# Performance work log

Hardware: AMD Instinct MI355X
Metric: run time of the kernel (lower is better)

## Reference

```python
import jax, jax.numpy as jnp
import numpy as np

N_NODES = 100000
N_EDGES = 1600000
IN_DIM = 128
HID_DIM = 128
N_MASK = 5000
N_CLASSES = 4


def gcn_layer(x, src, dst, edge_weight, W, b):
    """PyG GCNConv: x' = D^{-1/2} (A + I) D^{-1/2} (x W) + b, with edge weights."""
    n = x.shape[0]
    loop = jnp.arange(n, dtype=src.dtype)
    s = jnp.concatenate([src, loop])                      # [E+N]
    d = jnp.concatenate([dst, loop])                      # [E+N]
    w = jnp.concatenate([edge_weight, jnp.ones((n,), edge_weight.dtype)])
    deg = jax.ops.segment_sum(w, d, num_segments=n)       # weighted in-degree incl. self-loop
    dis = jnp.where(deg > 0, jax.lax.rsqrt(deg), 0.0)     # deg^{-1/2}, inf -> 0
    norm = dis[s] * w * dis[d]                            # [E+N]
    h = x @ W                                             # [N, H] small GEMM
    msg = h[s] * norm[:, None]                            # gather + scale  [E+N, H]
    out = jax.ops.segment_sum(msg, d, num_segments=n)     # scatter-add     [N, H]
    return out + b


def setup_inputs() -> dict:
    key = jax.random.key(0)
    ks = jax.random.split(key, 8)
    x = jax.random.normal(ks[0], (N_NODES, IN_DIM), dtype=jnp.float32)
    edge_weight = jax.random.uniform(ks[1], (N_EDGES,), dtype=jnp.float32)
    W1 = jax.random.normal(ks[2], (IN_DIM, HID_DIM), dtype=jnp.float32) * (1.0 / np.sqrt(IN_DIM))
    b1 = jnp.zeros((HID_DIM,), jnp.float32)
    W2 = jax.random.normal(ks[3], (HID_DIM, HID_DIM), dtype=jnp.float32) * (1.0 / np.sqrt(HID_DIM))
    b2 = jnp.zeros((HID_DIM,), jnp.float32)
    edge_index = jax.random.randint(ks[4], (2, N_EDGES), 0, N_NODES, dtype=jnp.int32)
    mask_idx = jax.random.randint(ks[5], (N_MASK,), 0, N_NODES, dtype=jnp.int32)
    y = jax.random.randint(ks[6], (N_NODES,), 0, N_CLASSES, dtype=jnp.int32)
    return {"x": x, "edge_weight": edge_weight, "W1": W1, "b1": b1,
            "W2": W2, "b2": b2, "edge_index": edge_index,
            "mask_idx": mask_idx, "y": y}


def reference(x, edge_weight, W1, b1, W2, b2, edge_index, mask_idx, y):
    src, dst = edge_index[0], edge_index[1]
    h = gcn_layer(x, src, dst, edge_weight, W1, b1)
    h = jax.nn.relu(h)
    # F.dropout(training=False) in eval mode is identity
    h = gcn_layer(h, src, dst, edge_weight, W2, b2)
    return h[mask_idx], y[mask_idx]
```

## Files before the change

kernel.cpp:

```cpp
#include <hip/hip_runtime.h>

constexpr int N = 100000;
constexpr int E = 1600000;
constexpr int D = 128;
constexpr int M = 5000;

constexpr int MF_BLKS = (N + 255) / 256;

constexpr int NBITS = 7;
constexpr int BUCKET = 1 << NBITS;
constexpr int NB  = (N + BUCKET - 1) / BUCKET;
constexpr int EB  = 2048;
constexpr int NPB = (E + EB - 1) / EB;
constexpr int EBP = 8192;
constexpr int NPP = (E + EBP - 1) / EBP;
constexpr int PREP_BLKS = 32;
constexpr int MB_BLKS = (M + 255) / 256;
constexpr int CAP = 3072;

typedef __attribute__((ext_vector_type(8))) short bf16x8;
typedef __attribute__((ext_vector_type(4))) float f32x4;


__device__ __forceinline__ unsigned int pack_bf16x2(float a, float b) {
    unsigned int ua = __float_as_uint(a);
    unsigned int ub = __float_as_uint(b);
    ua = (ua + 0x7FFFu + ((ua >> 16) & 1u)) >> 16;
    ub = (ub + 0x7FFFu + ((ub >> 16) & 1u)) & 0xFFFF0000u;
    return ua | ub;
}
__device__ __forceinline__ unsigned short bf16_rne(float a) {
    unsigned int ua = __float_as_uint(a);
    return (unsigned short)((ua + 0x7FFFu + ((ua >> 16) & 1u)) >> 16);
}
__device__ __forceinline__ float bf16_lo(unsigned int u) { return __uint_as_float(u << 16); }
__device__ __forceinline__ float bf16_hi(unsigned int u) { return __uint_as_float(u & 0xFFFF0000u); }


__global__ __launch_bounds__(256) void k_misc1(const int* __restrict__ dst,
                                               int* __restrict__ bucketCnt,
                                               const float* __restrict__ W1,
                                               unsigned int* __restrict__ Wt1,
                                               const int* __restrict__ mask,
                                               unsigned int* __restrict__ maskbit,
                                               unsigned int* __restrict__ needed) {
    __shared__ int h[NB];
    const int t = threadIdx.x;
    if (blockIdx.x < NPB) {
        for (int i = t; i < NB; i += 256) h[i] = 0;
        __syncthreads();
        const int base = blockIdx.x * EB;
#pragma unroll
        for (int i = 0; i < 8; ++i) {
            int e = base + t + i * 256;
            if (e < E) {
                int b = __builtin_nontemporal_load(dst + e) >> NBITS;
                atomicAdd(&h[b], 1);
            }
        }
        __syncthreads();
        for (int i = t; i < NB; i += 256) {
            int c = h[i];
            if (c) atomicAdd(&bucketCnt[i], c);
        }
    } else if (blockIdx.x < NPB + PREP_BLKS) {
        int idx = (blockIdx.x - NPB) * 256 + t;
        int n = idx >> 6, kk = idx & 63;
        float a = W1[(2 * kk) * D + n];
        float b = W1[(2 * kk + 1) * D + n];
        Wt1[idx] = pack_bf16x2(a, b);
    } else {
        int i = (blockIdx.x - NPB - PREP_BLKS) * 256 + t;
        if (i < M) {
            int n = mask[i];
            atomicOr(&maskbit[n >> 5], 1u << (n & 31));
            atomicOr(&needed[n >> 5], 1u << (n & 31));
        }
    }
}


__global__ __launch_bounds__(256) void k_misc2(const int* __restrict__ bucketCnt,
                                               int* __restrict__ bucketBase,
                                               int* __restrict__ gCursor,
                                               const unsigned int* __restrict__ maskbit,
                                               const int* __restrict__ src,
                                               const int* __restrict__ dst,
                                               unsigned int* __restrict__ needed) {
    const int t = threadIdx.x;
    if (blockIdx.x == 0) {
        __shared__ int waveS[4];
        const int lane = t & 63, wave = t >> 6;
        const int idx = t * 4;
        int c[4];
        int s = 0;
#pragma unroll
        for (int g = 0; g < 4; ++g) {
            c[g] = (idx + g < NB) ? bucketCnt[idx + g] : 0;
            s += c[g];
        }
        int v = s;
        for (int off = 1; off < 64; off <<= 1) {
            int u = __shfl_up(v, off);
            if (lane >= off) v += u;
        }
        if (lane == 63) waveS[wave] = v;
        __syncthreads();
        int wb = 0;
        for (int w = 0; w < 4; ++w) if (w < wave) wb += waveS[w];
        int run = wb + v - s;
#pragma unroll
        for (int g = 0; g < 4; ++g) {
            int pos = idx + g;
            if (pos < NB) {
                bucketBase[pos] = run;
                gCursor[pos] = run;
            }
            run += c[g];
        }
        if (t == 255) bucketBase[NB] = E;
    } else {
        const int base = (blockIdx.x - 1) * EB;
#pragma unroll
        for (int i = 0; i < 8; ++i) {
            int e = base + t + i * 256;
            if (e < E) {
                int d = __builtin_nontemporal_load(dst + e);
                if ((maskbit[d >> 5] >> (d & 31)) & 1u) {
                    int s = src[e];
                    atomicOr(&needed[s >> 5], 1u << (s & 31));
                }
            }
        }
    }
}


__global__ __launch_bounds__(1024) void k_part(const int* __restrict__ src,
                                               const int* __restrict__ dst,
                                               const float* __restrict__ ew,
                                               int* __restrict__ gCursor,
                                               unsigned long long* __restrict__ tmp) {
    __shared__ int cnt[NB];
    __shared__ int off[NB];
    __shared__ int rk[NB];
    const int t = threadIdx.x;
    for (int i = t; i < NB; i += 1024) { cnt[i] = 0; rk[i] = 0; }
    __syncthreads();

    const int eb = blockIdx.x * EBP;
    int d_[8], s_[8];
    float w_[8];
#pragma unroll
    for (int i = 0; i < 8; ++i) {
        int e = eb + t + i * 1024;
        if (e < E) {
            d_[i] = __builtin_nontemporal_load(dst + e);
            s_[i] = __builtin_nontemporal_load(src + e);
            w_[i] = __builtin_nontemporal_load(ew + e);
            atomicAdd(&cnt[d_[i] >> NBITS], 1);
        } else {
            d_[i] = -1;
        }
    }
    __syncthreads();

    for (int i = t; i < NB; i += 1024) {
        int c = cnt[i];
        if (c > 0) off[i] = atomicAdd(&gCursor[i], c);
    }
    __syncthreads();

#pragma unroll
    for (int i = 0; i < 8; ++i) {
        if (d_[i] >= 0) {
            int b = d_[i] >> NBITS;
            int r = atomicAdd(&rk[b], 1);
            unsigned long long rec =
                ((unsigned long long)(unsigned int)__float_as_int(w_[i]) << 32) |
                ((unsigned int)s_[i] << NBITS) | (unsigned int)(d_[i] & (BUCKET - 1));
            tmp[(size_t)off[b] + r] = rec;
        }
    }
}


union SMem {
    unsigned int Ws[128 * 68];
    struct { int cnt[BUCKET]; float wsum[BUCKET]; int waveS[2]; } l;
};


template <bool BF16IN>
__device__ __forceinline__ void gemm_mfma_body(unsigned int* __restrict__ Ws,
                                               const void* __restrict__ Xin,
                                               const unsigned int* __restrict__ Wt,
                                               unsigned short* __restrict__ out, int blk) {
    const int t = threadIdx.x;
#pragma unroll
    for (int i = 0; i < 8; ++i) {
        int f4 = t + i * 256;
        int n = f4 >> 4;
        int k4 = f4 & 15;
        uint4 w = ((const uint4*)Wt)[f4];
        *(uint4*)(&Ws[n * 68 + k4 * 4]) = w;
    }
    __syncthreads();

    const int wv = t >> 6, lane = t & 63;
    const int q = lane >> 4, l15 = lane & 15;
    const int rowBase = blk * 256 + wv * 64;

    f32x4 acc[4][8] = {};
#pragma unroll
    for (int kc = 0; kc < 4; ++kc) {
        bf16x8 af[4];
#pragma unroll
        for (int rt = 0; rt < 4; ++rt) {
            int row = rowBase + rt * 16 + l15;
            if (row > N - 1) row = N - 1;
            union { uint4 u; bf16x8 v; } cv;
            if (BF16IN) {
                cv.u = *(const uint4*)((const unsigned int*)Xin + (size_t)row * 64 + kc * 16 + q * 4);
            } else {
                const float* xr = (const float*)Xin + (size_t)row * D + kc * 32 + q * 8;
                float4 x0 = *(const float4*)xr;
                float4 x1 = *(const float4*)(xr + 4);
                cv.u.x = pack_bf16x2(x0.x, x0.y);
                cv.u.y = pack_bf16x2(x0.z, x0.w);
                cv.u.z = pack_bf16x2(x1.x, x1.y);
                cv.u.w = pack_bf16x2(x1.z, x1.w);
            }
            af[rt] = cv.v;
        }
#pragma unroll
        for (int ct = 0; ct < 8; ++ct) {
            union { uint4 u; bf16x8 v; } bv;
            bv.u = *(const uint4*)(&Ws[(ct * 16 + l15) * 68 + kc * 16 + q * 4]);
#pragma unroll
            for (int rt = 0; rt < 4; ++rt)
                acc[rt][ct] = __builtin_amdgcn_mfma_f32_16x16x32_bf16(af[rt], bv.v, acc[rt][ct], 0, 0, 0);
        }
    }

#pragma unroll
    for (int rt = 0; rt < 4; ++rt) {
#pragma unroll
        for (int ct = 0; ct < 8; ++ct) {
            int col = ct * 16 + l15;
#pragma unroll
            for (int r = 0; r < 4; ++r) {
                int row = rowBase + rt * 16 + q * 4 + r;
                if (row < N) out[(size_t)row * D + col] = bf16_rne(acc[rt][ct][r]);
            }
        }
    }
}


__device__ __forceinline__ void local_a_body(SMem& sm,
                                             const unsigned long long* __restrict__ tmp,
                                             const int* __restrict__ bucketBase,
                                             float* __restrict__ dis,
                                             int* __restrict__ offG) {
    const int b = blockIdx.x;
    const int t = threadIdx.x;
    const int segBeg = bucketBase[b];
    const int segEnd = bucketBase[b + 1];

    int*   cnt   = sm.l.cnt;
    float* wsum  = sm.l.wsum;
    int*   waveS = sm.l.waveS;
    if (t < BUCKET) { cnt[t] = 0; wsum[t] = 0.f; }
    __syncthreads();

    for (int e = segBeg + t; e < segEnd; e += 256) {
        unsigned long long rec = tmp[e];
        int dl = (int)(rec & (BUCKET - 1));
        float w = __uint_as_float((unsigned int)(rec >> 32));
        atomicAdd(&cnt[dl], 1);
        atomicAdd(&wsum[dl], w);
    }
    __syncthreads();

    const int lane = t & 63, wv = t >> 6;
    const int pv = (t < BUCKET) ? cnt[t] : 0;
    int v = pv;
    for (int o = 1; o < 64; o <<= 1) {
        int u = __shfl_up(v, o);
        if (lane >= o) v += u;
    }
    if (lane == 63 && wv < 2) waveS[wv] = v;
    __syncthreads();
    if (t < BUCKET) {
        const int wb = (wv == 1) ? waveS[0] : 0;
        const int ex = wb + v - pv;
        offG[b * BUCKET + t] = ex;
        const int node = b * BUCKET + t;
        if (node < N) dis[node] = rsqrtf(1.0f + wsum[t]);
    }
}


__global__ __launch_bounds__(256) void k_local_g1(const unsigned long long* __restrict__ tmp,
                                                  const int* __restrict__ bucketBase,
                                                  float* __restrict__ dis,
                                                  int* __restrict__ offG,
                                                  const float* __restrict__ x,
                                                  const unsigned int* __restrict__ Wt1,
                                                  unsigned short* __restrict__ A) {
    __shared__ SMem sm;
    if (blockIdx.x < NB) {
        local_a_body(sm, tmp, bucketBase, dis, offG);
    } else {
        gemm_mfma_body<false>(sm.Ws, x, Wt1, A, blockIdx.x - NB);
    }
}


__global__ __launch_bounds__(512) void k_sort_agg(const unsigned long long* __restrict__ tmp,
                                                  const int* __restrict__ bucketBase,
                                                  const int* __restrict__ offG,
                                                  const float* __restrict__ dis,
                                                  const unsigned int* __restrict__ needed,
                                                  const float* __restrict__ b,
                                                  const unsigned int* __restrict__ Hb,
                                                  int* __restrict__ rowStart,
                                                  int2* __restrict__ pairs,
                                                  unsigned int* __restrict__ outB) {
    __shared__ int2 lp[CAP];
    __shared__ int cnt[BUCKET];
    __shared__ int offL[BUCKET + 1];
    const int bk = blockIdx.x;
    const int t = threadIdx.x;
    const int segBeg = bucketBase[bk];
    const int segEnd = bucketBase[bk + 1];
    const int segLen = segEnd - segBeg;
    const bool fits = (segLen <= CAP);

    if (t < BUCKET) {
        int ex = offG[bk * BUCKET + t];
        offL[t] = ex;
        cnt[t] = 0;
        int node = bk * BUCKET + t;
        if (node < N) rowStart[node] = segBeg + ex;
    }
    if (t == 0) offL[BUCKET] = segLen;
    if (bk == NB - 1 && t == 0) rowStart[N] = E;
    __syncthreads();

    for (int e = segBeg + t; e < segEnd; e += 512) {
        unsigned long long rec = tmp[e];
        int dl = (int)(rec & (BUCKET - 1));
        int s  = (int)((rec >> NBITS) & 0xFFFFF);
        float w = __uint_as_float((unsigned int)(rec >> 32));
        float v = w * dis[s];
        int r = atomicAdd(&cnt[dl], 1);
        int pos = offL[dl] + r;
        int2 pr = make_int2(s, __float_as_int(v));
        pairs[segBeg + pos] = pr;
        if (fits) lp[pos] = pr;
    }
    __syncthreads();

    const int wv = t >> 6, lane = t & 63;
    for (int k = 0; k < 16; ++k) {
        const int nl = wv * 16 + k;
        const int node = bk * BUCKET + nl;
        if (node >= N) break;
        if (!((needed[node >> 5] >> (node & 31)) & 1u)) continue;
        const int beg = offL[nl], end = offL[nl + 1];
        float ax = 0.f, ay = 0.f;
        int j = beg;
        if (fits) {
            for (; j + 7 < end; j += 8) {
                int2 p[8];
                unsigned int h[8];
#pragma unroll
                for (int i = 0; i < 8; ++i) p[i] = lp[j + i];
#pragma unroll
                for (int i = 0; i < 8; ++i) h[i] = Hb[(size_t)p[i].x * 64 + lane];
#pragma unroll
                for (int i = 0; i < 8; ++i) {
                    float v = __int_as_float(p[i].y);
                    ax += bf16_lo(h[i]) * v;
                    ay += bf16_hi(h[i]) * v;
                }
            }
            for (; j < end; ++j) {
                int2 p0 = lp[j];
                unsigned int h0 = Hb[(size_t)p0.x * 64 + lane];
                float v0 = __int_as_float(p0.y);
                ax += bf16_lo(h0) * v0;
                ay += bf16_hi(h0) * v0;
            }
        } else {
            const int2* gp = pairs + segBeg;
            for (; j + 7 < end; j += 8) {
                int2 p[8];
                unsigned int h[8];
#pragma unroll
                for (int i = 0; i < 8; ++i) p[i] = gp[j + i];
#pragma unroll
                for (int i = 0; i < 8; ++i) h[i] = Hb[(size_t)p[i].x * 64 + lane];
#pragma unroll
                for (int i = 0; i < 8; ++i) {
                    float v = __int_as_float(p[i].y);
                    ax += bf16_lo(h[i]) * v;
                    ay += bf16_hi(h[i]) * v;
                }
            }
            for (; j < end; ++j) {
                int2 p0 = gp[j];
                unsigned int h0 = Hb[(size_t)p0.x * 64 + lane];
                float v0 = __int_as_float(p0.y);
                ax += bf16_lo(h0) * v0;
                ay += bf16_hi(h0) * v0;
            }
        }
        float dd = dis[node];
        float sn = dd * dd;
        unsigned int hs = Hb[(size_t)node * 64 + lane];
        float2 bb = ((const float2*)b)[lane];
        float ox = fmaxf(ax * dd + bf16_lo(hs) * sn + bb.x, 0.f);
        float oy = fmaxf(ay * dd + bf16_hi(hs) * sn + bb.y, 0.f);
        __builtin_nontemporal_store(pack_bf16x2(ox, oy), outB + (size_t)node * 64 + lane);
    }
}


__global__ __launch_bounds__(256) void k_mask_out(const unsigned int* __restrict__ Hb,
                                                  const int2* __restrict__ pairs,
                                                  const int* __restrict__ rowStart,
                                                  const float* __restrict__ dis,
                                                  const float* __restrict__ W2,
                                                  const float* __restrict__ b2,
                                                  const int* __restrict__ mask,
                                                  const int* __restrict__ y,
                                                  float* __restrict__ out) {
    __shared__ float w2s[64 * 132];
    __shared__ float rowL[4][128];
    const int t = threadIdx.x;
    const int wv = t >> 6, lane = t & 63;
    const int i = blockIdx.x * 4 + wv;
    const int node = mask[i];
    const int beg = rowStart[node], end = rowStart[node + 1];

    float ax = 0.f, ay = 0.f;
    int j = beg;
    for (; j + 7 < end; j += 8) {
        int2 p[8];
        unsigned int h[8];
#pragma unroll
        for (int ii = 0; ii < 8; ++ii) p[ii] = pairs[j + ii];
#pragma unroll
        for (int ii = 0; ii < 8; ++ii) h[ii] = Hb[(size_t)p[ii].x * 64 + lane];
#pragma unroll
        for (int ii = 0; ii < 8; ++ii) {
            float v = __int_as_float(p[ii].y);
            ax += bf16_lo(h[ii]) * v;
            ay += bf16_hi(h[ii]) * v;
        }
    }
    for (; j < end; ++j) {
        int2 p0 = pairs[j];
        unsigned int h0 = Hb[(size_t)p0.x * 64 + lane];
        float v0 = __int_as_float(p0.y);
        ax += bf16_lo(h0) * v0;
        ay += bf16_hi(h0) * v0;
    }
    {
        float dd = dis[node];
        float sn = dd * dd;
        unsigned int hs = Hb[(size_t)node * 64 + lane];
        rowL[wv][2 * lane]     = ax * dd + bf16_lo(hs) * sn;
        rowL[wv][2 * lane + 1] = ay * dd + bf16_hi(hs) * sn;
    }

    float2 bb = ((const float2*)b2)[lane];
    float acc0 = bb.x, acc1 = bb.y;
#pragma unroll
    for (int h0 = 0; h0 < 2; ++h0) {
        __syncthreads();
        for (int idx = t; idx < 2048; idx += 256) {
            float4 v = ((const float4*)W2)[h0 * 2048 + idx];
            int k = (idx * 4) >> 7, n = (idx * 4) & 127;
            *(float4*)(&w2s[k * 132 + n]) = v;
        }
        __syncthreads();
#pragma unroll 8
        for (int k = 0; k < 64; ++k) {
            float a = rowL[wv][h0 * 64 + k];
            float2 w = *(const float2*)(&w2s[k * 132 + 2 * lane]);
            acc0 += a * w.x;
            acc1 += a * w.y;
        }
    }
    ((float2*)(out + (size_t)i * D))[lane] = make_float2(acc0, acc1);
    if (lane == 0) out[(size_t)M * D + i] = (float)y[node];
}

extern "C" void kernel_launch(void* const* d_in, const int* in_sizes, int n_in,
                              void* d_out, int out_size, void* d_ws, size_t ws_size,
                              hipStream_t stream) {
    const float* x  = (const float*)d_in[0];
    const float* ew = (const float*)d_in[1];
    const float* W1 = (const float*)d_in[2];
    const float* b1 = (const float*)d_in[3];
    const float* W2 = (const float*)d_in[4];
    const float* b2 = (const float*)d_in[5];
    const int* eidx = (const int*)d_in[6];
    const int* mask = (const int*)d_in[7];
    const int* y    = (const int*)d_in[8];
    const int* src = eidx;
    const int* dst = eidx + E;

    char* ws = (char*)d_ws;
    float* dis      = (float*)(ws);
    int*   rowStart = (int*)(ws + (size_t)512 * 1024);
    unsigned int* maskbit = (unsigned int*)(ws + (size_t)960 * 1024);
    unsigned int* needed  = (unsigned int*)(ws + (size_t)976 * 1024);
    int*   bucketCnt  = (int*)(ws + (size_t)992 * 1024);
    int*   bucketBase = (int*)(ws + (size_t)996 * 1024);
    int*   gCursor    = (int*)(ws + (size_t)1000 * 1024);
    unsigned int* Wt1 = (unsigned int*)(ws + (size_t)1008 * 1024);
    int*   offG     = (int*)(ws + (size_t)1040 * 1024);
    int2*  pairs    = (int2*)(ws + (size_t)2 * 1024 * 1024);
    unsigned long long* tmp = (unsigned long long*)(ws + (size_t)16 * 1024 * 1024);
    unsigned short* A  = (unsigned short*)(ws + (size_t)29 * 1024 * 1024);
    unsigned short* B  = (unsigned short*)(ws + (size_t)55 * 1024 * 1024);

    (void)hipMemsetAsync(ws + (size_t)960 * 1024, 0, (size_t)40 * 1024, stream);
    hipLaunchKernelGGL(k_misc1, dim3(NPB + PREP_BLKS + MB_BLKS), dim3(256), 0, stream,
                       dst, bucketCnt, W1, Wt1, mask, maskbit, needed);

    hipLaunchKernelGGL(k_misc2, dim3(1 + NPB), dim3(256), 0, stream,
                       bucketCnt, bucketBase, gCursor, maskbit, src, dst, needed);

    hipLaunchKernelGGL(k_part, dim3(NPP), dim3(1024), 0, stream,
                       src, dst, ew, gCursor, tmp);

    hipLaunchKernelGGL(k_local_g1, dim3(NB + MF_BLKS), dim3(256), 0, stream,
                       tmp, bucketBase, dis, offG, x, Wt1, A);

    hipLaunchKernelGGL(k_sort_agg, dim3(NB), dim3(512), 0, stream,
                       tmp, bucketBase, offG, dis, needed, b1,
                       (const unsigned int*)A, rowStart, pairs, (unsigned int*)B);

    hipLaunchKernelGGL(k_mask_out, dim3(M / 4), dim3(256), 0, stream,
                       (const unsigned int*)B, pairs, rowStart, dis, W2, b2,
                       mask, y, (float*)d_out);
}
```

Baseline: 276.0 us.

## Fold needed-set marking into partition, write pairs only for masked nodes, dynamic worklist

Moves the masked-destination 'needed' bit marking out of a separate full-edge pass and into the partition kernel, which already holds dst and src in registers, so the scan becomes a single-block kernel. In the sort/aggregate kernel, edge pairs are written to global memory only for masked destination nodes (or when the bucket overflows shared memory), which cuts global store traffic. Needed nodes are compacted into a shared worklist that waves pull from dynamically, which balances load. The trade-off is extra atomics and maskbit lookups in k_part, plus a shared-memory atomic per node fetch.

```diff
diff --git a/kernel.cpp b/kernel.cpp
--- a/kernel.cpp
+++ b/kernel.cpp
@@ -80,59 +80,40 @@
 }
 
 
-__global__ __launch_bounds__(256) void k_misc2(const int* __restrict__ bucketCnt,
-                                               int* __restrict__ bucketBase,
-                                               int* __restrict__ gCursor,
-                                               const unsigned int* __restrict__ maskbit,
-                                               const int* __restrict__ src,
-                                               const int* __restrict__ dst,
-                                               unsigned int* __restrict__ needed) {
-    const int t = threadIdx.x;
-    if (blockIdx.x == 0) {
-        __shared__ int waveS[4];
-        const int lane = t & 63, wave = t >> 6;
-        const int idx = t * 4;
-        int c[4];
-        int s = 0;
-#pragma unroll
-        for (int g = 0; g < 4; ++g) {
-            c[g] = (idx + g < NB) ? bucketCnt[idx + g] : 0;
-            s += c[g];
-        }
-        int v = s;
-        for (int off = 1; off < 64; off <<= 1) {
-            int u = __shfl_up(v, off);
-            if (lane >= off) v += u;
-        }
-        if (lane == 63) waveS[wave] = v;
-        __syncthreads();
-        int wb = 0;
-        for (int w = 0; w < 4; ++w) if (w < wave) wb += waveS[w];
-        int run = wb + v - s;
-#pragma unroll
-        for (int g = 0; g < 4; ++g) {
-            int pos = idx + g;
-            if (pos < NB) {
-                bucketBase[pos] = run;
-                gCursor[pos] = run;
-            }
-            run += c[g];
-        }
-        if (t == 255) bucketBase[NB] = E;
-    } else {
-        const int base = (blockIdx.x - 1) * EB;
-#pragma unroll
-        for (int i = 0; i < 8; ++i) {
-            int e = base + t + i * 256;
-            if (e < E) {
-                int d = __builtin_nontemporal_load(dst + e);
-                if ((maskbit[d >> 5] >> (d & 31)) & 1u) {
-                    int s = src[e];
-                    atomicOr(&needed[s >> 5], 1u << (s & 31));
-                }
-            }
-        }
-    }
+__global__ __launch_bounds__(256) void k_scan(const int* __restrict__ bucketCnt,
+                                              int* __restrict__ bucketBase,
+                                              int* __restrict__ gCursor) {
+    __shared__ int waveS[4];
+    const int t = threadIdx.x;
+    const int lane = t & 63, wave = t >> 6;
+    const int idx = t * 4;
+    int c[4];
+    int s = 0;
+#pragma unroll
+    for (int g = 0; g < 4; ++g) {
+        c[g] = (idx + g < NB) ? bucketCnt[idx + g] : 0;
+        s += c[g];
+    }
+    int v = s;
+    for (int off = 1; off < 64; off <<= 1) {
+        int u = __shfl_up(v, off);
+        if (lane >= off) v += u;
+    }
+    if (lane == 63) waveS[wave] = v;
+    __syncthreads();
+    int wb = 0;
+    for (int w = 0; w < 4; ++w) if (w < wave) wb += waveS[w];
+    int run = wb + v - s;
+#pragma unroll
+    for (int g = 0; g < 4; ++g) {
+        int pos = idx + g;
+        if (pos < NB) {
+            bucketBase[pos] = run;
+            gCursor[pos] = run;
+        }
+        run += c[g];
+    }
+    if (t == 255) bucketBase[NB] = E;
 }
 
 
@@ -140,7 +121,9 @@
                                                const int* __restrict__ dst,
                                                const float* __restrict__ ew,
                                                int* __restrict__ gCursor,
-                                               unsigned long long* __restrict__ tmp) {
+                                               unsigned long long* __restrict__ tmp,
+                                               const unsigned int* __restrict__ maskbit,
+                                               unsigned int* __restrict__ needed) {
     __shared__ int cnt[NB];
     __shared__ int off[NB];
     __shared__ int rk[NB];
@@ -180,6 +163,8 @@
                 ((unsigned long long)(unsigned int)__float_as_int(w_[i]) << 32) |
                 ((unsigned int)s_[i] << NBITS) | (unsigned int)(d_[i] & (BUCKET - 1));
             tmp[(size_t)off[b] + r] = rec;
+            if ((maskbit[d_[i] >> 5] >> (d_[i] & 31)) & 1u)
+                atomicOr(&needed[s_[i] >> 5], 1u << (s_[i] & 31));
         }
     }
 }
@@ -323,6 +308,7 @@
                                                   const int* __restrict__ offG,
                                                   const float* __restrict__ dis,
                                                   const unsigned int* __restrict__ needed,
+                                                  const unsigned int* __restrict__ maskbit,
                                                   const float* __restrict__ b,
                                                   const unsigned int* __restrict__ Hb,
                                                   int* __restrict__ rowStart,
@@ -331,6 +317,8 @@
     __shared__ int2 lp[CAP];
     __shared__ int cnt[BUCKET];
     __shared__ int offL[BUCKET + 1];
+    __shared__ int wl[BUCKET];
+    __shared__ int nw, wcur;
     const int bk = blockIdx.x;
     const int t = threadIdx.x;
     const int segBeg = bucketBase[bk];
@@ -338,15 +326,23 @@
     const int segLen = segEnd - segBeg;
     const bool fits = (segLen <= CAP);
 
+    if (t == 0) { nw = 0; wcur = 0; offL[BUCKET] = segLen; }
+    __syncthreads();
     if (t < BUCKET) {
         int ex = offG[bk * BUCKET + t];
         offL[t] = ex;
         cnt[t] = 0;
         int node = bk * BUCKET + t;
-        if (node < N) rowStart[node] = segBeg + ex;
-    }
-    if (t == 0) offL[BUCKET] = segLen;
+        if (node < N) {
+            rowStart[node] = segBeg + ex;
+            if ((needed[node >> 5] >> (node & 31)) & 1u) {
+                int r = atomicAdd(&nw, 1);
+                wl[r] = t;
+            }
+        }
+    }
     if (bk == NB - 1 && t == 0) rowStart[N] = E;
+    const uint4 mb4 = ((const uint4*)maskbit)[bk];
     __syncthreads();
 
     for (int e = segBeg + t; e < segEnd; e += 512) {
@@ -358,17 +354,20 @@
         int r = atomicAdd(&cnt[dl], 1);
         int pos = offL[dl] + r;
         int2 pr = make_int2(s, __float_as_int(v));
-        pairs[segBeg + pos] = pr;
+        unsigned int mw = (dl < 32) ? mb4.x : (dl < 64) ? mb4.y : (dl < 96) ? mb4.z : mb4.w;
+        if (((mw >> (dl & 31)) & 1u) || !fits) pairs[segBeg + pos] = pr;
         if (fits) lp[pos] = pr;
     }
     __syncthreads();
 
-    const int wv = t >> 6, lane = t & 63;
-    for (int k = 0; k < 16; ++k) {
-        const int nl = wv * 16 + k;
+    const int lane = t & 63;
+    for (;;) {
+        int idx;
+        if (lane == 0) idx = atomicAdd(&wcur, 1);
+        idx = __shfl(idx, 0);
+        if (idx >= nw) break;
+        const int nl = wl[idx];
         const int node = bk * BUCKET + nl;
-        if (node >= N) break;
-        if (!((needed[node >> 5] >> (node & 31)) & 1u)) continue;
         const int beg = offL[nl], end = offL[nl + 1];
         float ax = 0.f, ay = 0.f;
         int j = beg;
@@ -534,17 +533,17 @@
     hipLaunchKernelGGL(k_misc1, dim3(NPB + PREP_BLKS + MB_BLKS), dim3(256), 0, stream,
                        dst, bucketCnt, W1, Wt1, mask, maskbit, needed);
 
-    hipLaunchKernelGGL(k_misc2, dim3(1 + NPB), dim3(256), 0, stream,
-                       bucketCnt, bucketBase, gCursor, maskbit, src, dst, needed);
+    hipLaunchKernelGGL(k_scan, dim3(1), dim3(256), 0, stream,
+                       bucketCnt, bucketBase, gCursor);
 
     hipLaunchKernelGGL(k_part, dim3(NPP), dim3(1024), 0, stream,
-                       src, dst, ew, gCursor, tmp);
+                       src, dst, ew, gCursor, tmp, maskbit, needed);
 
     hipLaunchKernelGGL(k_local_g1, dim3(NB + MF_BLKS), dim3(256), 0, stream,
                        tmp, bucketBase, dis, offG, x, Wt1, A);
 
     hipLaunchKernelGGL(k_sort_agg, dim3(NB), dim3(512), 0, stream,
-                       tmp, bucketBase, offG, dis, needed, b1,
+                       tmp, bucketBase, offG, dis, needed, maskbit, b1,
                        (const unsigned int*)A, rowStart, pairs, (unsigned int*)B);
 
     hipLaunchKernelGGL(k_mask_out, dim3(M / 4), dim3(256), 0, stream,
```

Result: faster. 257.6 us (-6.7%).
